# Kernel tuning notes

Measured on AMD Instinct MI355X. Metric: run time of the kernel, lower is better.

The kernel has to match this reference:

```python
import jax, jax.numpy as jnp
import numpy as np

N = 50000
E = 600000
IN = 128
H = 4
F = 32  # per-head out; concat output = H*F = 128
NEG_SLOPE = 0.2


def setup_inputs() -> dict:
    key = jax.random.key(0)
    k1, k2, k3, k4, k5, k6 = jax.random.split(key, 6)
    x = jax.random.normal(k1, (N, IN), dtype=jnp.float32)
    edge_index = jax.random.randint(k2, (2, E), 0, N, dtype=jnp.int64)
    W = jax.random.normal(k3, (IN, H * F), dtype=jnp.float32) * 0.05
    att_src = jax.random.normal(k4, (H, F), dtype=jnp.float32) * 0.05
    att_dst = jax.random.normal(k5, (H, F), dtype=jnp.float32) * 0.05
    bias = jnp.zeros((H * F,), dtype=jnp.float32)
    return {"x": x, "edge_index": edge_index, "W": W,
            "att_src": att_src, "att_dst": att_dst, "bias": bias}


def reference(x, edge_index, W, att_src, att_dst, bias):
    n = x.shape[0]
    # add self loops (PyG GATConv default)
    loop = jnp.arange(n, dtype=edge_index.dtype)
    src = jnp.concatenate([edge_index[0], loop])
    dst = jnp.concatenate([edge_index[1], loop])

    h = (x @ W).reshape(n, H, F)                      # [N,H,F]
    a_s = jnp.einsum('nhf,hf->nh', h, att_src)        # [N,H]
    a_d = jnp.einsum('nhf,hf->nh', h, att_dst)        # [N,H]

    e = a_s[src] + a_d[dst]                           # [E',H]
    e = jax.nn.leaky_relu(e, NEG_SLOPE)
    # segment softmax over incoming edges of each destination node
    m = jax.ops.segment_max(e, dst, num_segments=n)   # [N,H]
    m = jnp.where(jnp.isfinite(m), m, 0.0)
    ex = jnp.exp(e - m[dst])                          # [E',H]
    denom = jax.ops.segment_sum(ex, dst, num_segments=n)  # [N,H]
    alpha = ex / denom[dst]                           # [E',H]

    msgs = alpha[:, :, None] * h[src]                 # [E',H,F]
    out = jax.ops.segment_sum(msgs, dst, num_segments=n)  # [N,H,F]
    out = out.reshape(n, H * F) + bias
    return jax.nn.relu(out)
```

## Files before the change

kernel.cpp:

```cpp
#include <hip/hip_runtime.h>

#define NEG_SLOPE 0.2f
#define CAP 64
#define NB 256
#define MAXB 4096
#define A_EDGES 2048
#define A_BLOCKS 293
#define GEMM_BLOCKS 782

typedef __attribute__((ext_vector_type(8))) short short8;
typedef __attribute__((ext_vector_type(4))) float f32x4;

__device__ __forceinline__ unsigned short f2bf(float f) {
    union { float f; unsigned int i; } v; v.f = f;
    unsigned int r = v.i + 0x7FFF + ((v.i >> 16) & 1);
    return (unsigned short)(r >> 16);
}
__device__ __forceinline__ float lrelu(float v) {
    return v > 0.f ? v : NEG_SLOPE * v;
}

__global__ void gat_prep(const float* __restrict__ W,
                         const float* __restrict__ att_src,
                         const float* __restrict__ att_dst,
                         unsigned short* __restrict__ wt,
                         int* __restrict__ bcur)
{
    int i = blockIdx.x * blockDim.x + threadIdx.x;
    if (i < NB) bcur[i] = 0;
    if (i >= 144 * 128) return;
    int r = i >> 7, k = i & 127;
    float v = 0.f;
    if (r < 128) {
        v = W[k * 128 + r];
    } else if (r < 136) {
        int hh = (r - 128) & 3;
        const float* att = (r < 132) ? att_src : att_dst;
        float s = 0.f;
        #pragma unroll 8
        for (int f = 0; f < 32; f++)
            s = fmaf(W[k * 128 + hh * 32 + f], att[hh * 32 + f], s);
        v = s;
    }
    wt[i] = f2bf(v);
}

__global__ __launch_bounds__(256) void gat_mega(
    const float* __restrict__ x, const unsigned short* __restrict__ wt,
    const int* __restrict__ ei, unsigned short* __restrict__ hb,
    float* __restrict__ a_s, float* __restrict__ a_d,
    int* __restrict__ bcur, unsigned int* __restrict__ bbuf, int nE, int n)
{
    const int bid = blockIdx.x;
    if (bid < A_BLOCKS) {
        __shared__ int hist[NB];
        __shared__ int gbase[NB];
        const int tid = threadIdx.x;
        hist[tid] = 0;
        __syncthreads();

        int base = bid * A_EDGES + tid * 8;
        int sreg[8], dreg[8], rreg[8];
        bool act = (base + 8 <= nE);
        if (act) {
            int4 s0 = ((const int4*)(ei + base))[0];
            int4 s1 = ((const int4*)(ei + base))[1];
            int4 d0 = ((const int4*)(ei + nE + base))[0];
            int4 d1 = ((const int4*)(ei + nE + base))[1];
            sreg[0]=s0.x; sreg[1]=s0.y; sreg[2]=s0.z; sreg[3]=s0.w;
            sreg[4]=s1.x; sreg[5]=s1.y; sreg[6]=s1.z; sreg[7]=s1.w;
            dreg[0]=d0.x; dreg[1]=d0.y; dreg[2]=d0.z; dreg[3]=d0.w;
            dreg[4]=d1.x; dreg[5]=d1.y; dreg[6]=d1.z; dreg[7]=d1.w;
            #pragma unroll
            for (int j = 0; j < 8; j++)
                rreg[j] = atomicAdd(&hist[dreg[j] >> 8], 1);
        }
        __syncthreads();
        {
            int h = hist[tid];
            gbase[tid] = (h > 0) ? atomicAdd(&bcur[tid], h) : 0;
        }
        __syncthreads();
        if (act) {
            #pragma unroll
            for (int j = 0; j < 8; j++) {
                int b = dreg[j] >> 8;
                int idx = gbase[b] + rreg[j];
                if (idx < MAXB)
                    bbuf[(size_t)b * MAXB + idx] =
                        ((unsigned int)dreg[j] << 16) | (unsigned int)sreg[j];
            }
        }
        return;
    }
    const int wave = threadIdx.x >> 6, lane = threadIdx.x & 63;
    const int quad = lane >> 4, l15 = lane & 15;
    const int m0 = (bid - A_BLOCKS) * 64 + wave * 16;
    if (m0 >= n) return;
    const int row = m0 + l15;

    f32x4 acc[9];
    #pragma unroll
    for (int t = 0; t < 9; t++) acc[t] = (f32x4){0.f, 0.f, 0.f, 0.f};

    const float* xr = x + (size_t)row * 128 + quad * 8;
    #pragma unroll
    for (int kk = 0; kk < 4; ++kk) {
        float4 f0 = ((const float4*)(xr + kk * 32))[0];
        float4 f1 = ((const float4*)(xr + kk * 32))[1];
        short8 afrag;
        afrag[0] = (short)f2bf(f0.x); afrag[1] = (short)f2bf(f0.y);
        afrag[2] = (short)f2bf(f0.z); afrag[3] = (short)f2bf(f0.w);
        afrag[4] = (short)f2bf(f1.x); afrag[5] = (short)f2bf(f1.y);
        afrag[6] = (short)f2bf(f1.z); afrag[7] = (short)f2bf(f1.w);
        #pragma unroll
        for (int t = 0; t < 9; ++t) {
            short8 bfrag = *(const short8*)(wt + (size_t)(t * 16 + l15) * 128 + kk * 32 + quad * 8);
            acc[t] = __builtin_amdgcn_mfma_f32_16x16x32_bf16(afrag, bfrag, acc[t], 0, 0, 0);
        }
    }

    #pragma unroll
    for (int t = 0; t < 8; ++t)
        #pragma unroll
        for (int r = 0; r < 4; ++r) {
            int orow = m0 + quad * 4 + r;
            hb[(size_t)orow * 128 + t * 16 + l15] = f2bf(acc[t][r]);
        }
    if (l15 < 8) {
        float* dst = (l15 < 4) ? a_s : a_d;
        int hh = l15 & 3;
        #pragma unroll
        for (int r = 0; r < 4; ++r) {
            int orow = m0 + quad * 4 + r;
            dst[(size_t)orow * 4 + hh] = acc[8][r];
        }
    }
}

__global__ __launch_bounds__(256) void gat_ell_build(
    const int* __restrict__ bcur, const unsigned int* __restrict__ bbuf,
    unsigned short* __restrict__ csr, int* __restrict__ cnt, int n)
{
    __shared__ int lcnt[NB];
    const int b = blockIdx.x, tid = threadIdx.x;
    lcnt[tid] = 0;
    __syncthreads();
    int count = min(bcur[b], MAXB);
    for (int i = tid; i < count; i += 256) {
        unsigned int u = bbuf[(size_t)b * MAXB + i];
        int d = (int)(u >> 16);
        int slot = atomicAdd(&lcnt[d & 255], 1);
        if (slot < CAP)
            csr[(size_t)d * CAP + slot] = (unsigned short)(u & 0xFFFFu);
    }
    __syncthreads();
    int d = (b << 8) + tid;
    if (d < n) cnt[d] = lcnt[tid];
}

__global__ __launch_bounds__(256) void gat_accumulate(
    const int* __restrict__ cnt, const unsigned short* __restrict__ csr,
    const float4* __restrict__ a_s4, const float4* __restrict__ a_d4,
    const uint4* __restrict__ h4, const float* __restrict__ bias,
    float* __restrict__ out, int n)
{
    __shared__ float wtab[4][256];
    __shared__ int   stab[4][64];
    int lane = threadIdx.x & 63;
    int wslot = threadIdx.x >> 6;
    int d = blockIdx.x * 4 + wslot;
    if (d >= n) return;

    int deg  = min(cnt[d], CAP - 1);
    int degi = deg + 1;
    int slotv = (lane < deg) ? (int)csr[(size_t)d * CAP + lane] : d;
    stab[wslot][lane] = slotv;

    float4 ad = a_d4[d];
    float4 w4 = {0.f, 0.f, 0.f, 0.f};
    if (lane < degi) {
        float4 as = a_s4[slotv];
        w4.x = __expf(lrelu(as.x + ad.x));
        w4.y = __expf(lrelu(as.y + ad.y));
        w4.z = __expf(lrelu(as.z + ad.z));
        w4.w = __expf(lrelu(as.w + ad.w));
    }
    ((float4*)wtab[wslot])[lane] = w4;

    int quad = lane >> 4, c = lane & 15;
    int head = c >> 2;
    const float* wrow = wtab[wslot];
    const int*   srow = stab[wslot];

    float acc[8] = {0.f,0.f,0.f,0.f,0.f,0.f,0.f,0.f};
    float den = 0.f;

    for (int j = 0; j < degi; j += 16) {
        int je[4]; int sv[4]; uint4 hv[4];
        #pragma unroll
        for (int u = 0; u < 4; u++) {
            je[u] = j + 4 * u + quad;
            sv[u] = srow[je[u]];
        }
        #pragma unroll
        for (int u = 0; u < 4; u++)
            hv[u] = h4[(size_t)sv[u] * 16 + c];
        #pragma unroll
        for (int u = 0; u < 4; u++) {
            float w = wrow[je[u] * 4 + head];
            union { unsigned int i; float f; } lo, hi;
            #pragma unroll
            for (int k = 0; k < 4; k++) {
                unsigned int uu = (&hv[u].x)[k];
                lo.i = uu << 16; hi.i = uu & 0xFFFF0000u;
                acc[2*k]   = fmaf(w, lo.f, acc[2*k]);
                acc[2*k+1] = fmaf(w, hi.f, acc[2*k+1]);
            }
            den += w;
        }
    }

    #pragma unroll
    for (int m = 16; m <= 32; m <<= 1) {
        #pragma unroll
        for (int k = 0; k < 8; k++) acc[k] += __shfl_xor(acc[k], m);
        den += __shfl_xor(den, m);
    }

    if (quad == 0) {
        float inv = 1.f / den;
        float4 b0 = ((const float4*)bias)[2*c];
        float4 b1 = ((const float4*)bias)[2*c + 1];
        float4 o0, o1;
        o0.x = fmaxf(acc[0]*inv + b0.x, 0.f); o0.y = fmaxf(acc[1]*inv + b0.y, 0.f);
        o0.z = fmaxf(acc[2]*inv + b0.z, 0.f); o0.w = fmaxf(acc[3]*inv + b0.w, 0.f);
        o1.x = fmaxf(acc[4]*inv + b1.x, 0.f); o1.y = fmaxf(acc[5]*inv + b1.y, 0.f);
        o1.z = fmaxf(acc[6]*inv + b1.z, 0.f); o1.w = fmaxf(acc[7]*inv + b1.w, 0.f);
        ((float4*)out)[(size_t)d * 32 + 2*c]     = o0;
        ((float4*)out)[(size_t)d * 32 + 2*c + 1] = o1;
    }
}

extern "C" void kernel_launch(void* const* d_in, const int* in_sizes, int n_in,
                              void* d_out, int out_size, void* d_ws, size_t ws_size,
                              hipStream_t stream)
{
    const float* x       = (const float*)d_in[0];
    const int*   ei      = (const int*)d_in[1];
    const float* W       = (const float*)d_in[2];
    const float* att_src = (const float*)d_in[3];
    const float* att_dst = (const float*)d_in[4];
    const float* bias    = (const float*)d_in[5];

    const int n  = in_sizes[0] / 128;
    const int nE = in_sizes[1] / 2;

    char* wsb = (char*)d_ws;
    unsigned short* hb  = (unsigned short*)wsb;
    unsigned short* wt  = hb + (size_t)n * 128;
    float* a_s = (float*)(wt + 144 * 128);
    float* a_d = a_s + (size_t)n * 4;
    int*   cnt  = (int*)(a_d + (size_t)n * 4);
    int*   bcur = cnt + n;
    unsigned short* csr = (unsigned short*)(bcur + NB);
    unsigned int*  bbuf = (unsigned int*)(csr + (size_t)n * CAP);
    float* out = (float*)d_out;

    const int nbkt = (n + 255) >> 8;

    gat_prep<<<(144 * 128 + 255) / 256, 256, 0, stream>>>(W, att_src, att_dst,
                                                          wt, bcur);
    gat_mega<<<A_BLOCKS + GEMM_BLOCKS, 256, 0, stream>>>(x, wt, ei, hb, a_s,
                                                         a_d, bcur, bbuf, nE, n);
    gat_ell_build<<<nbkt, 256, 0, stream>>>(bcur, bbuf, csr, cnt, n);
    gat_accumulate<<<(n + 3) / 4, 256, 0, stream>>>(cnt, csr, (const float4*)a_s,
                                                    (const float4*)a_d,
                                                    (const uint4*)hb, bias, out, n);
}
```

Before: 147.4 us.

## Fuse ELL bucket build into accumulate kernel using shared-memory adjacency

Merges the per-bucket ELL construction and the attention-weighted aggregation into one kernel. Each 1024-thread block builds its 256-node adjacency in LDS and then has 16 waves process those destinations. This removes a kernel launch and the global csr/cnt write-and-read round trip. In exchange, the grid shrinks to one block per bucket (fewer blocks than CUs) with heavy LDS use, which reduces parallelism and latency hiding for the gather phase.

```diff
diff --git a/kernel.cpp b/kernel.cpp
--- a/kernel.cpp
+++ b/kernel.cpp
@@ -138,107 +138,102 @@
     }
 }
 
-__global__ __launch_bounds__(256) void gat_ell_build(
+__global__ __launch_bounds__(1024) void gat_bucket_acc(
     const int* __restrict__ bcur, const unsigned int* __restrict__ bbuf,
-    unsigned short* __restrict__ csr, int* __restrict__ cnt, int n)
-{
-    __shared__ int lcnt[NB];
-    const int b = blockIdx.x, tid = threadIdx.x;
-    lcnt[tid] = 0;
-    __syncthreads();
-    int count = min(bcur[b], MAXB);
-    for (int i = tid; i < count; i += 256) {
-        unsigned int u = bbuf[(size_t)b * MAXB + i];
-        int d = (int)(u >> 16);
-        int slot = atomicAdd(&lcnt[d & 255], 1);
-        if (slot < CAP)
-            csr[(size_t)d * CAP + slot] = (unsigned short)(u & 0xFFFFu);
-    }
-    __syncthreads();
-    int d = (b << 8) + tid;
-    if (d < n) cnt[d] = lcnt[tid];
-}
-
-__global__ __launch_bounds__(256) void gat_accumulate(
-    const int* __restrict__ cnt, const unsigned short* __restrict__ csr,
     const float4* __restrict__ a_s4, const float4* __restrict__ a_d4,
     const uint4* __restrict__ h4, const float* __restrict__ bias,
     float* __restrict__ out, int n)
 {
-    __shared__ float wtab[4][256];
-    __shared__ int   stab[4][64];
-    int lane = threadIdx.x & 63;
-    int wslot = threadIdx.x >> 6;
-    int d = blockIdx.x * 4 + wslot;
-    if (d >= n) return;
-
-    int deg  = min(cnt[d], CAP - 1);
-    int degi = deg + 1;
-    int slotv = (lane < deg) ? (int)csr[(size_t)d * CAP + lane] : d;
-    stab[wslot][lane] = slotv;
-
-    float4 ad = a_d4[d];
-    float4 w4 = {0.f, 0.f, 0.f, 0.f};
-    if (lane < degi) {
-        float4 as = a_s4[slotv];
-        w4.x = __expf(lrelu(as.x + ad.x));
-        w4.y = __expf(lrelu(as.y + ad.y));
-        w4.z = __expf(lrelu(as.z + ad.z));
-        w4.w = __expf(lrelu(as.w + ad.w));
-    }
-    ((float4*)wtab[wslot])[lane] = w4;
-
-    int quad = lane >> 4, c = lane & 15;
-    int head = c >> 2;
-    const float* wrow = wtab[wslot];
-    const int*   srow = stab[wslot];
-
-    float acc[8] = {0.f,0.f,0.f,0.f,0.f,0.f,0.f,0.f};
-    float den = 0.f;
-
-    for (int j = 0; j < degi; j += 16) {
-        int je[4]; int sv[4]; uint4 hv[4];
-        #pragma unroll
-        for (int u = 0; u < 4; u++) {
-            je[u] = j + 4 * u + quad;
-            sv[u] = srow[je[u]];
-        }
-        #pragma unroll
-        for (int u = 0; u < 4; u++)
-            hv[u] = h4[(size_t)sv[u] * 16 + c];
-        #pragma unroll
-        for (int u = 0; u < 4; u++) {
-            float w = wrow[je[u] * 4 + head];
-            union { unsigned int i; float f; } lo, hi;
-            #pragma unroll
-            for (int k = 0; k < 4; k++) {
-                unsigned int uu = (&hv[u].x)[k];
-                lo.i = uu << 16; hi.i = uu & 0xFFFF0000u;
-                acc[2*k]   = fmaf(w, lo.f, acc[2*k]);
-                acc[2*k+1] = fmaf(w, hi.f, acc[2*k+1]);
+    __shared__ int lcnt[NB];
+    __shared__ unsigned short lcsr[NB][CAP];
+    __shared__ float wtab[16][256];
+    __shared__ int   stab[16][64];
+    const int b = blockIdx.x, tid = threadIdx.x;
+
+    if (tid < NB) lcnt[tid] = 0;
+    __syncthreads();
+    int count = min(bcur[b], MAXB);
+    for (int i = tid; i < count; i += 1024) {
+        unsigned int u = bbuf[(size_t)b * MAXB + i];
+        int ld = (int)((u >> 16) & 255);
+        int slot = atomicAdd(&lcnt[ld], 1);
+        if (slot < CAP) lcsr[ld][slot] = (unsigned short)(u & 0xFFFFu);
+    }
+    __syncthreads();
+
+    const int wv = tid >> 6, lane = tid & 63;
+    const int quad = lane >> 4, c = lane & 15;
+    const int head = c >> 2;
+    const float4 b0 = ((const float4*)bias)[2 * c];
+    const float4 b1 = ((const float4*)bias)[2 * c + 1];
+    const float* wrow = wtab[wv];
+    const int*   srow = stab[wv];
+
+    for (int ld = wv; ld < 256; ld += 16) {
+        int d = (b << 8) + ld;
+        if (d >= n) break;
+
+        int deg  = min(lcnt[ld], CAP - 1);
+        int degi = deg + 1;
+        int slotv = (lane < deg) ? (int)lcsr[ld][lane] : d;
+        stab[wv][lane] = slotv;
+
+        float4 ad = a_d4[d];
+        float4 w4 = {0.f, 0.f, 0.f, 0.f};
+        if (lane < degi) {
+            float4 as = a_s4[slotv];
+            w4.x = __expf(lrelu(as.x + ad.x));
+            w4.y = __expf(lrelu(as.y + ad.y));
+            w4.z = __expf(lrelu(as.z + ad.z));
+            w4.w = __expf(lrelu(as.w + ad.w));
+        }
+        ((float4*)wtab[wv])[lane] = w4;
+
+        float acc[8] = {0.f,0.f,0.f,0.f,0.f,0.f,0.f,0.f};
+        float den = 0.f;
+
+        for (int j = 0; j < degi; j += 16) {
+            int je[4]; int sv[4]; uint4 hv[4];
+            #pragma unroll
+            for (int u = 0; u < 4; u++) {
+                je[u] = j + 4 * u + quad;
+                sv[u] = srow[je[u]];
             }
-            den += w;
-        }
-    }
-
-    #pragma unroll
-    for (int m = 16; m <= 32; m <<= 1) {
-        #pragma unroll
-        for (int k = 0; k < 8; k++) acc[k] += __shfl_xor(acc[k], m);
-        den += __shfl_xor(den, m);
-    }
-
-    if (quad == 0) {
-        float inv = 1.f / den;
-        float4 b0 = ((const float4*)bias)[2*c];
-        float4 b1 = ((const float4*)bias)[2*c + 1];
-        float4 o0, o1;
-        o0.x = fmaxf(acc[0]*inv + b0.x, 0.f); o0.y = fmaxf(acc[1]*inv + b0.y, 0.f);
-        o0.z = fmaxf(acc[2]*inv + b0.z, 0.f); o0.w = fmaxf(acc[3]*inv + b0.w, 0.f);
-        o1.x = fmaxf(acc[4]*inv + b1.x, 0.f); o1.y = fmaxf(acc[5]*inv + b1.y, 0.f);
-        o1.z = fmaxf(acc[6]*inv + b1.z, 0.f); o1.w = fmaxf(acc[7]*inv + b1.w, 0.f);
-        ((float4*)out)[(size_t)d * 32 + 2*c]     = o0;
-        ((float4*)out)[(size_t)d * 32 + 2*c + 1] = o1;
+            #pragma unroll
+            for (int u = 0; u < 4; u++)
+                hv[u] = h4[(size_t)sv[u] * 16 + c];
+            #pragma unroll
+            for (int u = 0; u < 4; u++) {
+                float w = wrow[je[u] * 4 + head];
+                union { unsigned int i; float f; } lo, hi;
+                #pragma unroll
+                for (int k = 0; k < 4; k++) {
+                    unsigned int uu = (&hv[u].x)[k];
+                    lo.i = uu << 16; hi.i = uu & 0xFFFF0000u;
+                    acc[2*k]   = fmaf(w, lo.f, acc[2*k]);
+                    acc[2*k+1] = fmaf(w, hi.f, acc[2*k+1]);
+                }
+                den += w;
+            }
+        }
+
+        #pragma unroll
+        for (int m = 16; m <= 32; m <<= 1) {
+            #pragma unroll
+            for (int k = 0; k < 8; k++) acc[k] += __shfl_xor(acc[k], m);
+            den += __shfl_xor(den, m);
+        }
+
+        if (quad == 0) {
+            float inv = 1.f / den;
+            float4 o0, o1;
+            o0.x = fmaxf(acc[0]*inv + b0.x, 0.f); o0.y = fmaxf(acc[1]*inv + b0.y, 0.f);
+            o0.z = fmaxf(acc[2]*inv + b0.z, 0.f); o0.w = fmaxf(acc[3]*inv + b0.w, 0.f);
+            o1.x = fmaxf(acc[4]*inv + b1.x, 0.f); o1.y = fmaxf(acc[5]*inv + b1.y, 0.f);
+            o1.z = fmaxf(acc[6]*inv + b1.z, 0.f); o1.w = fmaxf(acc[7]*inv + b1.w, 0.f);
+            ((float4*)out)[(size_t)d * 32 + 2*c]     = o0;
+            ((float4*)out)[(size_t)d * 32 + 2*c + 1] = o1;
+        }
     }
 }
 
@@ -261,10 +256,8 @@
     unsigned short* wt  = hb + (size_t)n * 128;
     float* a_s = (float*)(wt + 144 * 128);
     float* a_d = a_s + (size_t)n * 4;
-    int*   cnt  = (int*)(a_d + (size_t)n * 4);
-    int*   bcur = cnt + n;
-    unsigned short* csr = (unsigned short*)(bcur + NB);
-    unsigned int*  bbuf = (unsigned int*)(csr + (size_t)n * CAP);
+    int*   bcur = (int*)(a_d + (size_t)n * 4);
+    unsigned int* bbuf = (unsigned int*)(bcur + NB);
     float* out = (float*)d_out;
 
     const int nbkt = (n + 255) >> 8;
@@ -273,8 +266,7 @@
                                                           wt, bcur);
     gat_mega<<<A_BLOCKS + GEMM_BLOCKS, 256, 0, stream>>>(x, wt, ei, hb, a_s,
                                                          a_d, bcur, bbuf, nE, n);
-    gat_ell_build<<<nbkt, 256, 0, stream>>>(bcur, bbuf, csr, cnt, n);
-    gat_accumulate<<<(n + 3) / 4, 256, 0, stream>>>(cnt, csr, (const float4*)a_s,
-                                                    (const float4*)a_d,
-                                                    (const uint4*)hb, bias, out, n);
-}
+    gat_bucket_acc<<<nbkt, 1024, 0, stream>>>(bcur, bbuf, (const float4*)a_s,
+                                              (const float4*)a_d,
+                                              (const uint4*)hb, bias, out, n);
+}
```

New measurement: 148.5 us. No clear change (+0.8%).
